# Kernel tuning notes

Hardware: AMD Instinct MI355X
Metric: run time of the kernel (lower is better)

The kernel has to match this reference:

```python
import jax, jax.numpy as jnp
import numpy as np

N_NODES = 100000
N_EDGES = 1600000
IN_CH = 128
HID = 128
OUT_CH = 2
NUM_GRAPHS = 512


def _mlp_params(key, d_in, d_out):
    k1, k2 = jax.random.split(key)
    s1 = 1.0 / np.sqrt(d_in)
    s2 = 1.0 / np.sqrt(d_out)
    return (jax.random.uniform(k1, (d_in, d_out), jnp.float32, -s1, s1),
            jnp.zeros((d_out,), jnp.float32),
            jax.random.uniform(k2, (d_out, d_out), jnp.float32, -s2, s2),
            jnp.zeros((d_out,), jnp.float32))


def setup_inputs() -> dict:
    key = jax.random.key(0)
    ks = jax.random.split(key, 8)
    x = jax.random.normal(ks[0], (N_NODES, IN_CH), jnp.float32)
    edge_index = jax.random.randint(ks[1], (2, N_EDGES), 0, N_NODES, jnp.int64)
    batch = jnp.sort(jax.random.randint(ks[2], (N_NODES,), 0, NUM_GRAPHS, jnp.int64))
    w1_0, b1_0, w2_0, b2_0 = _mlp_params(ks[3], IN_CH, HID)
    w1_1, b1_1, w2_1, b2_1 = _mlp_params(ks[4], HID, HID)
    w1_2, b1_2, w2_2, b2_2 = _mlp_params(ks[5], HID, HID)
    s = 1.0 / np.sqrt(HID)
    w_lin = jax.random.uniform(ks[6], (HID, OUT_CH), jnp.float32, -s, s)
    b_lin = jnp.zeros((OUT_CH,), jnp.float32)
    return {"x": x, "edge_index": edge_index, "batch": batch,
            "w1_0": w1_0, "b1_0": b1_0, "w2_0": w2_0, "b2_0": b2_0,
            "w1_1": w1_1, "b1_1": b1_1, "w2_1": w2_1, "b2_1": b2_1,
            "w1_2": w1_2, "b1_2": b1_2, "w2_2": w2_2, "b2_2": b2_2,
            "w_lin": w_lin, "b_lin": b_lin}


def _gin_conv(x, src, dst, w1, b1, w2, b2):
    # GINConv with eps=0: MLP(x + sum_{j in N(i)} x_j)
    agg = jax.ops.segment_sum(x[src], dst, num_segments=N_NODES)  # [N, d]
    h = x + agg
    h = jax.nn.relu(h @ w1 + b1)
    return h @ w2 + b2


def reference(x, edge_index, batch,
              w1_0, b1_0, w2_0, b2_0,
              w1_1, b1_1, w2_1, b2_1,
              w1_2, b1_2, w2_2, b2_2,
              w_lin, b_lin):
    src, dst = edge_index[0], edge_index[1]
    h = _gin_conv(x, src, dst, w1_0, b1_0, w2_0, b2_0)
    h = jax.nn.relu(h)
    h = jax.nn.relu(_gin_conv(h, src, dst, w1_1, b1_1, w2_1, b2_1))
    h = jax.nn.relu(h)  # forward applies relu twice after GIN1
    h = _gin_conv(h, src, dst, w1_2, b1_2, w2_2, b2_2)
    # global mean pool per graph
    sums = jax.ops.segment_sum(h, batch, num_segments=NUM_GRAPHS)  # [G, d]
    counts = jax.ops.segment_sum(jnp.ones((N_NODES,), h.dtype), batch,
                                 num_segments=NUM_GRAPHS)
    pooled = sums / jnp.maximum(counts, 1.0)[:, None]
    # dropout is identity in eval mode
    return pooled @ w_lin + b_lin  # [G, OUT_CH]
```

## Files before the change

kernel.cpp:

```cpp
#include <hip/hip_runtime.h>
#include <hip/hip_bf16.h>

#define N_NODES   100000
#define N_EDGES   1600000
#define IN_CH     128
#define HID       128
#define OUT_CH    2
#define NUM_GRAPHS 512

#define BKT_SHIFT 9
#define NB2 ((N_NODES + 511) >> BKT_SHIFT)
#define PB  200
#define CHUNK (N_EDGES / PB)

#define NCAST (N_NODES * IN_CH / 4 / 256)

typedef __attribute__((ext_vector_type(8))) short bf16x8;
typedef __attribute__((ext_vector_type(4))) float f32x4;
typedef unsigned int uint32;
typedef unsigned long long uint64;

static __device__ __forceinline__ float b2f(uint32 b) {
    return __uint_as_float(b << 16);
}
static __device__ __forceinline__ unsigned short f2b(float f) {
    uint32 u = __float_as_uint(f);
    u += 0x7fffu + ((u >> 16) & 1u);
    return (unsigned short)(u >> 16);
}
static __device__ __forceinline__ void acc8(float* a, int4 v) {
    uint32 x;
    x = (uint32)v.x; a[0] += __uint_as_float(x << 16); a[1] += __uint_as_float(x & 0xffff0000u);
    x = (uint32)v.y; a[2] += __uint_as_float(x << 16); a[3] += __uint_as_float(x & 0xffff0000u);
    x = (uint32)v.z; a[4] += __uint_as_float(x << 16); a[5] += __uint_as_float(x & 0xffff0000u);
    x = (uint32)v.w; a[6] += __uint_as_float(x << 16); a[7] += __uint_as_float(x & 0xffff0000u);
}

__global__ void k_front(const float* __restrict__ x, unsigned short* __restrict__ h,
                        const float* w0, const float* w1, const float* w2,
                        const float* w3, const float* w4, const float* w5,
                        unsigned short* __restrict__ wt,
                        const int* __restrict__ dst, int* __restrict__ histG) {
    __shared__ int hist[NB2];
    int bid = blockIdx.x, t = threadIdx.x;
    if (bid < NCAST) {
        int base = (bid * 256 + t) * 4;
        float4 v = *(const float4*)(x + base);
        ushort4 o;
        o.x = f2b(v.x); o.y = f2b(v.y); o.z = f2b(v.z); o.w = f2b(v.w);
        *(ushort4*)(h + base) = o;
    } else if (bid < NCAST + 6) {
        const float* ws[6] = {w0, w1, w2, w3, w4, w5};
        int wi = bid - NCAST;
        const float* w = ws[wi];
        unsigned short* o = wt + wi * 16384;
        for (int i = t; i < 16384; i += 256) {
            int k = i >> 7, n = i & 127;
            o[n * 128 + k] = f2b(w[i]);
        }
    } else {
        int blk = bid - NCAST - 6;
        for (int i = t; i < NB2; i += 256) hist[i] = 0;
        __syncthreads();
        int base = blk * CHUNK;
        for (int i = t; i < CHUNK; i += 256)
            atomicAdd(&hist[dst[base + i] >> BKT_SHIFT], 1);
        __syncthreads();
        for (int i = t; i < NB2; i += 256) histG[i * PB + blk] = hist[i];
    }
}

__global__ void k_scan1(const int* __restrict__ in, int* __restrict__ out,
                        int* __restrict__ bsum, int n) {
    __shared__ int sm[256];
    int b = blockIdx.x, t = threadIdx.x;
    int base = b * 1024 + t * 4;
    int v0 = 0, v1 = 0, v2 = 0, v3 = 0;
    if (base + 3 < n) {
        int4 q = *(const int4*)(in + base);
        v0 = q.x; v1 = q.y; v2 = q.z; v3 = q.w;
    } else {
        if (base + 0 < n) v0 = in[base + 0];
        if (base + 1 < n) v1 = in[base + 1];
        if (base + 2 < n) v2 = in[base + 2];
        if (base + 3 < n) v3 = in[base + 3];
    }
    int s = v0 + v1 + v2 + v3;
    sm[t] = s;
    __syncthreads();
    for (int off = 1; off < 256; off <<= 1) {
        int u = (t >= off) ? sm[t - off] : 0;
        __syncthreads();
        sm[t] += u;
        __syncthreads();
    }
    int p = (t == 0) ? 0 : sm[t - 1];
    int o0 = p, o1 = p + v0, o2 = o1 + v1, o3 = o2 + v2;
    if (base + 3 < n) {
        *(int4*)(out + base) = make_int4(o0, o1, o2, o3);
    } else {
        if (base + 0 < n) out[base + 0] = o0;
        if (base + 1 < n) out[base + 1] = o1;
        if (base + 2 < n) out[base + 2] = o2;
        if (base + 3 < n) out[base + 3] = o3;
    }
    if (t == 255) bsum[b] = s + ((t == 0) ? 0 : sm[t - 1]);
}

__global__ void k_scan3b(int* __restrict__ out, const int* __restrict__ bsum, int n) {
    __shared__ int add_s;
    int b = blockIdx.x, t = threadIdx.x;
    if (t == 0) {
        int s = 0;
        for (int i = 0; i < b; ++i) s += bsum[i];
        add_s = s;
    }
    __syncthreads();
    int add = add_s;
    int base = b * 1024 + t * 4;
    if (base + 3 < n) {
        int4 q = *(const int4*)(out + base);
        q.x += add; q.y += add; q.z += add; q.w += add;
        *(int4*)(out + base) = q;
    } else {
        for (int j = 0; j < 4; ++j)
            if (base + j < n) out[base + j] += add;
    }
}

__global__ void k_p3g(const int* __restrict__ ei, const int* __restrict__ baseG,
                      uint64* __restrict__ ebuf,
                      const int* __restrict__ batch, int* __restrict__ goff) {
    __shared__ int cur[NB2];
    int t = threadIdx.x, blk = blockIdx.x;
    if (blk >= PB) {
        int g = (blk - PB) * 512 + t;
        if (g <= NUM_GRAPHS) {
            int lo = 0, hi = N_NODES;
            while (lo < hi) {
                int mid = (lo + hi) >> 1;
                if (batch[mid] < g) lo = mid + 1; else hi = mid;
            }
            goff[g] = lo;
        }
        return;
    }
    for (int i = t; i < NB2; i += 512) cur[i] = baseG[i * PB + blk];
    __syncthreads();
    int base = blk * CHUNK;
    for (int i = t; i < CHUNK; i += 512) {
        int e = base + i;
        int src = ei[e];
        int dst = ei[N_EDGES + e];
        int pos = atomicAdd(&cur[dst >> BKT_SHIFT], 1);
        ebuf[pos] = ((uint64)(uint32)dst << 32) | (uint32)src;
    }
}

__global__ void k_p4(const uint64* __restrict__ ebuf, const int* __restrict__ baseG,
                     int* __restrict__ off, int* __restrict__ csr) {
    __shared__ int ldeg[512];
    __shared__ int lscan[512];
    __shared__ int lcur[512];
    int b = blockIdx.x, t = threadIdx.x;
    int node0 = b << BKT_SHIFT;
    int nn = min(512, N_NODES - node0);
    int e0 = baseG[b * PB];
    int e1 = (b == NB2 - 1) ? N_EDGES : baseG[(b + 1) * PB];
    ldeg[t] = 0;
    __syncthreads();
    for (int e = e0 + t; e < e1; e += 512) {
        int dst = (int)(ebuf[e] >> 32);
        atomicAdd(&ldeg[dst - node0], 1);
    }
    __syncthreads();
    lscan[t] = ldeg[t];
    __syncthreads();
    for (int o = 1; o < 512; o <<= 1) {
        int v = (t >= o) ? lscan[t - o] : 0;
        __syncthreads();
        lscan[t] += v;
        __syncthreads();
    }
    int excl = (t == 0) ? 0 : lscan[t - 1];
    lcur[t] = e0 + excl;
    if (t < nn) off[node0 + t] = e0 + excl;
    if (b == NB2 - 1 && t == 0) off[N_NODES] = N_EDGES;
    __syncthreads();
    for (int e = e0 + t; e < e1; e += 512) {
        uint64 pr = ebuf[e];
        int dst = (int)(pr >> 32);
        int pos = atomicAdd(&lcur[dst - node0], 1);
        csr[pos] = (int)(pr & 0xffffffffu);
    }
}

__global__ void k_agg(const unsigned short* __restrict__ h,
                      const int* __restrict__ off, const int* __restrict__ csr,
                      unsigned short* __restrict__ hs) {
    int wid = (blockIdx.x * 256 + threadIdx.x) >> 6;
    int lane = threadIdx.x & 63;
    if (wid >= N_NODES) return;
    int g = lane >> 4, sub = lane & 15;
    int e0 = off[wid], e1 = off[wid + 1];
    float a[8] = {0.f, 0.f, 0.f, 0.f, 0.f, 0.f, 0.f, 0.f};
    int e = e0 + g;
    for (; e + 12 < e1; e += 16) {
        int s0 = csr[e], s1 = csr[e + 4], s2 = csr[e + 8], s3 = csr[e + 12];
        int4 v0 = *(const int4*)(h + (size_t)s0 * 128 + sub * 8);
        int4 v1 = *(const int4*)(h + (size_t)s1 * 128 + sub * 8);
        int4 v2 = *(const int4*)(h + (size_t)s2 * 128 + sub * 8);
        int4 v3 = *(const int4*)(h + (size_t)s3 * 128 + sub * 8);
        acc8(a, v0); acc8(a, v1); acc8(a, v2); acc8(a, v3);
    }
    for (; e + 4 < e1; e += 8) {
        int s0 = csr[e];
        int s1 = csr[e + 4];
        int4 v0 = *(const int4*)(h + (size_t)s0 * 128 + sub * 8);
        int4 v1 = *(const int4*)(h + (size_t)s1 * 128 + sub * 8);
        acc8(a, v0);
        acc8(a, v1);
    }
    if (e < e1) {
        int s0 = csr[e];
        int4 v0 = *(const int4*)(h + (size_t)s0 * 128 + sub * 8);
        acc8(a, v0);
    }
#pragma unroll
    for (int j = 0; j < 8; ++j) {
        a[j] += __shfl_xor(a[j], 16);
        a[j] += __shfl_xor(a[j], 32);
    }
    if (g == 0) {
        int4 sv = *(const int4*)(h + (size_t)wid * 128 + sub * 8);
        acc8(a, sv);
        int4 o;
        o.x = (int)((uint32)f2b(a[0]) | ((uint32)f2b(a[1]) << 16));
        o.y = (int)((uint32)f2b(a[2]) | ((uint32)f2b(a[3]) << 16));
        o.z = (int)((uint32)f2b(a[4]) | ((uint32)f2b(a[5]) << 16));
        o.w = (int)((uint32)f2b(a[6]) | ((uint32)f2b(a[7]) << 16));
        *(int4*)(hs + (size_t)wid * 128 + sub * 8) = o;
    }
}

template<int OUTER_RELU>
__global__ void k_mlp(const unsigned short* __restrict__ hs,
                      const unsigned short* __restrict__ w1t, const float* __restrict__ b1,
                      const unsigned short* __restrict__ w2t, const float* __restrict__ b2,
                      unsigned short* __restrict__ ho) {
    __shared__ unsigned short T[32 * 128];
    int tid = threadIdx.x;
    int lane = tid & 63, wave = tid >> 6;
    int l15 = lane & 15, l4 = lane >> 4;
    int row0 = blockIdx.x * 32;
    int wn0 = wave * 32;

    bf16x8 w1f[2][4], w2f[2][4];
#pragma unroll
    for (int nt = 0; nt < 2; ++nt)
#pragma unroll
        for (int k = 0; k < 4; ++k) {
            int o = (wn0 + nt * 16 + l15) * 128 + k * 32 + l4 * 8;
            w1f[nt][k] = *(const bf16x8*)(w1t + o);
            w2f[nt][k] = *(const bf16x8*)(w2t + o);
        }
    float bias1[2] = { b1[wn0 + l15], b1[wn0 + 16 + l15] };
    float bias2[2] = { b2[wn0 + l15], b2[wn0 + 16 + l15] };

#pragma unroll
    for (int mt = 0; mt < 2; ++mt) {
        int arow = row0 + mt * 16 + l15;
        const unsigned short* ap = hs + (size_t)arow * 128 + l4 * 8;
        bf16x8 a0 = *(const bf16x8*)(ap);
        bf16x8 a1 = *(const bf16x8*)(ap + 32);
        bf16x8 a2 = *(const bf16x8*)(ap + 64);
        bf16x8 a3 = *(const bf16x8*)(ap + 96);
#pragma unroll
        for (int nt = 0; nt < 2; ++nt) {
            f32x4 acc = {0.f, 0.f, 0.f, 0.f};
            acc = __builtin_amdgcn_mfma_f32_16x16x32_bf16(a0, w1f[nt][0], acc, 0, 0, 0);
            acc = __builtin_amdgcn_mfma_f32_16x16x32_bf16(a1, w1f[nt][1], acc, 0, 0, 0);
            acc = __builtin_amdgcn_mfma_f32_16x16x32_bf16(a2, w1f[nt][2], acc, 0, 0, 0);
            acc = __builtin_amdgcn_mfma_f32_16x16x32_bf16(a3, w1f[nt][3], acc, 0, 0, 0);
#pragma unroll
            for (int j = 0; j < 4; ++j) {
                float v = fmaxf(acc[j] + bias1[nt], 0.f);
                int trow = mt * 16 + l4 * 4 + j;
                int tcol = wn0 + nt * 16 + l15;
                int byte = (trow * 256 + tcol * 2) ^ ((trow & 7) << 4);
                *(unsigned short*)((char*)T + byte) = f2b(v);
            }
        }
    }
    __syncthreads();

#pragma unroll
    for (int mt = 0; mt < 2; ++mt) {
        int trow = mt * 16 + l15;
        int sw = (trow & 7) << 4;
        int rb = trow * 256 + l4 * 16;
        bf16x8 t0 = *(const bf16x8*)((const char*)T + ((rb + 0)   ^ sw));
        bf16x8 t1 = *(const bf16x8*)((const char*)T + ((rb + 64)  ^ sw));
        bf16x8 t2 = *(const bf16x8*)((const char*)T + ((rb + 128) ^ sw));
        bf16x8 t3 = *(const bf16x8*)((const char*)T + ((rb + 192) ^ sw));
        __syncthreads();
#pragma unroll
        for (int nt = 0; nt < 2; ++nt) {
            f32x4 acc = {0.f, 0.f, 0.f, 0.f};
            acc = __builtin_amdgcn_mfma_f32_16x16x32_bf16(t0, w2f[nt][0], acc, 0, 0, 0);
            acc = __builtin_amdgcn_mfma_f32_16x16x32_bf16(t1, w2f[nt][1], acc, 0, 0, 0);
            acc = __builtin_amdgcn_mfma_f32_16x16x32_bf16(t2, w2f[nt][2], acc, 0, 0, 0);
            acc = __builtin_amdgcn_mfma_f32_16x16x32_bf16(t3, w2f[nt][3], acc, 0, 0, 0);
#pragma unroll
            for (int j = 0; j < 4; ++j) {
                float v = acc[j] + bias2[nt];
                if (OUTER_RELU) v = fmaxf(v, 0.f);
                int orow = mt * 16 + l4 * 4 + j;
                int ocol = wn0 + nt * 16 + l15;
                int byte = (orow * 256 + ocol * 2) ^ ((orow & 7) << 4);
                *(unsigned short*)((char*)T + byte) = f2b(v);
            }
        }
    }
    __syncthreads();

    for (int c = tid; c < 512; c += 256) {
        int r = c >> 4, cc = c & 15;
        int byte = (r * 256 + cc * 16) ^ ((r & 7) << 4);
        int4 v = *(const int4*)((const char*)T + byte);
        *(int4*)(ho + (size_t)(row0 + r) * 128 + cc * 8) = v;
    }
}

__global__ void k_pool(const unsigned short* __restrict__ h,
                       const int* __restrict__ goff,
                       const float* __restrict__ wl, const float* __restrict__ bl,
                       float* __restrict__ out) {
    __shared__ float sm[4][64][2];
    int g = blockIdx.x;
    int tid = threadIdx.x;
    int wave = tid >> 6, lane = tid & 63;
    int e0 = goff[g], e1 = goff[g + 1];
    int c2 = lane << 1;
    float s0 = 0.f, s1 = 0.f;
    int r = e0 + wave;
    for (; r + 4 < e1; r += 8) {
        uint32 v0 = *(const uint32*)(h + (size_t)r * 128 + c2);
        uint32 v1 = *(const uint32*)(h + (size_t)(r + 4) * 128 + c2);
        s0 += b2f(v0 & 0xffffu) + b2f(v1 & 0xffffu);
        s1 += b2f(v0 >> 16) + b2f(v1 >> 16);
    }
    if (r < e1) {
        uint32 v = *(const uint32*)(h + (size_t)r * 128 + c2);
        s0 += b2f(v & 0xffffu);
        s1 += b2f(v >> 16);
    }
    sm[wave][lane][0] = s0;
    sm[wave][lane][1] = s1;
    __syncthreads();
    if (wave == 0) {
        s0 = sm[0][lane][0] + sm[1][lane][0] + sm[2][lane][0] + sm[3][lane][0];
        s1 = sm[0][lane][1] + sm[1][lane][1] + sm[2][lane][1] + sm[3][lane][1];
        float inv = 1.f / fmaxf((float)(e1 - e0), 1.f);
        s0 *= inv; s1 *= inv;
        float o0 = s0 * wl[c2 * 2]     + s1 * wl[(c2 + 1) * 2];
        float o1 = s0 * wl[c2 * 2 + 1] + s1 * wl[(c2 + 1) * 2 + 1];
#pragma unroll
        for (int d = 32; d; d >>= 1) {
            o0 += __shfl_down(o0, d);
            o1 += __shfl_down(o1, d);
        }
        if (lane == 0) {
            out[g * 2]     = o0 + bl[0];
            out[g * 2 + 1] = o1 + bl[1];
        }
    }
}

extern "C" void kernel_launch(void* const* d_in, const int* in_sizes, int n_in,
                              void* d_out, int out_size, void* d_ws, size_t ws_size,
                              hipStream_t stream) {
    const float* x     = (const float*)d_in[0];
    const int*   ei    = (const int*)d_in[1];
    const int*   batch = (const int*)d_in[2];
    const float* w1[3] = {(const float*)d_in[3],  (const float*)d_in[7],  (const float*)d_in[11]};
    const float* b1[3] = {(const float*)d_in[4],  (const float*)d_in[8],  (const float*)d_in[12]};
    const float* w2[3] = {(const float*)d_in[5],  (const float*)d_in[9],  (const float*)d_in[13]};
    const float* b2[3] = {(const float*)d_in[6],  (const float*)d_in[10], (const float*)d_in[14]};
    const float* wl    = (const float*)d_in[15];
    const float* bl    = (const float*)d_in[16];

    char* p = (char*)d_ws;
    auto alloc = [&](size_t bytes) {
        char* r = p;
        p += (bytes + 255) & ~(size_t)255;
        return r;
    };
    int* off    = (int*)alloc((size_t)(N_NODES + 1) * 4);
    int* goff   = (int*)alloc((size_t)(NUM_GRAPHS + 1) * 4);
    int* histG  = (int*)alloc((size_t)(NB2 * PB) * 4);
    int* baseG  = (int*)alloc((size_t)(NB2 * PB + 1) * 4);
    int* bsum   = (int*)alloc((size_t)128 * 4);
    int* csr    = (int*)alloc((size_t)N_EDGES * 4);
    unsigned short* wts = (unsigned short*)alloc((size_t)6 * 16384 * 2);
    unsigned short* hA  = (unsigned short*)alloc((size_t)N_NODES * 128 * 2);
    unsigned short* hS  = (unsigned short*)alloc((size_t)N_NODES * 128 * 2);
    unsigned short* hB  = (unsigned short*)alloc((size_t)N_NODES * 128 * 2);
    uint64* ebuf = (uint64*)hS;

    k_front<<<NCAST + 6 + PB, 256, 0, stream>>>(x, hA,
        w1[0], w2[0], w1[1], w2[1], w1[2], w2[2], wts, ei + N_EDGES, histG);

    const int SCAN_N = NB2 * PB;
    const int SCAN_BLOCKS = (SCAN_N + 1023) / 1024;
    k_scan1<<<SCAN_BLOCKS, 256, 0, stream>>>(histG, baseG, bsum, SCAN_N);
    k_scan3b<<<SCAN_BLOCKS, 256, 0, stream>>>(baseG, bsum, SCAN_N);
    k_p3g<<<PB + 2, 512, 0, stream>>>(ei, baseG, ebuf, batch, goff);
    k_p4<<<NB2, 512, 0, stream>>>(ebuf, baseG, off, csr);

    unsigned short* wt1[3] = {wts,             wts + 2 * 16384, wts + 4 * 16384};
    unsigned short* wt2[3] = {wts + 1 * 16384, wts + 3 * 16384, wts + 5 * 16384};

    const int AGG_GRID = N_NODES / 4;
    const int MLP_GRID = N_NODES / 32;

    k_agg<<<AGG_GRID, 256, 0, stream>>>(hA, off, csr, hS);
    k_mlp<1><<<MLP_GRID, 256, 0, stream>>>(hS, wt1[0], b1[0], wt2[0], b2[0], hB);
    k_agg<<<AGG_GRID, 256, 0, stream>>>(hB, off, csr, hS);
    k_mlp<1><<<MLP_GRID, 256, 0, stream>>>(hS, wt1[1], b1[1], wt2[1], b2[1], hA);
    k_agg<<<AGG_GRID, 256, 0, stream>>>(hA, off, csr, hS);
    k_mlp<0><<<MLP_GRID, 256, 0, stream>>>(hS, wt1[2], b1[2], wt2[2], b2[2], hB);

    k_pool<<<NUM_GRAPHS, 256, 0, stream>>>(hB, goff, wl, bl, (float*)d_out);
}
```

Baseline: 375.9 us.

## Fuse neighbor aggregation into GIN MLP kernel via shared-memory tile

```diff
diff --git a/kernel.cpp b/kernel.cpp
--- a/kernel.cpp
+++ b/kernel.cpp
@@ -195,66 +195,64 @@
     }
 }
 
-__global__ void k_agg(const unsigned short* __restrict__ h,
+template<int OUTER_RELU>
+__global__ void k_gin(const unsigned short* __restrict__ h,
                       const int* __restrict__ off, const int* __restrict__ csr,
-                      unsigned short* __restrict__ hs) {
-    int wid = (blockIdx.x * 256 + threadIdx.x) >> 6;
-    int lane = threadIdx.x & 63;
-    if (wid >= N_NODES) return;
-    int g = lane >> 4, sub = lane & 15;
-    int e0 = off[wid], e1 = off[wid + 1];
-    float a[8] = {0.f, 0.f, 0.f, 0.f, 0.f, 0.f, 0.f, 0.f};
-    int e = e0 + g;
-    for (; e + 12 < e1; e += 16) {
-        int s0 = csr[e], s1 = csr[e + 4], s2 = csr[e + 8], s3 = csr[e + 12];
-        int4 v0 = *(const int4*)(h + (size_t)s0 * 128 + sub * 8);
-        int4 v1 = *(const int4*)(h + (size_t)s1 * 128 + sub * 8);
-        int4 v2 = *(const int4*)(h + (size_t)s2 * 128 + sub * 8);
-        int4 v3 = *(const int4*)(h + (size_t)s3 * 128 + sub * 8);
-        acc8(a, v0); acc8(a, v1); acc8(a, v2); acc8(a, v3);
-    }
-    for (; e + 4 < e1; e += 8) {
-        int s0 = csr[e];
-        int s1 = csr[e + 4];
-        int4 v0 = *(const int4*)(h + (size_t)s0 * 128 + sub * 8);
-        int4 v1 = *(const int4*)(h + (size_t)s1 * 128 + sub * 8);
-        acc8(a, v0);
-        acc8(a, v1);
-    }
-    if (e < e1) {
-        int s0 = csr[e];
-        int4 v0 = *(const int4*)(h + (size_t)s0 * 128 + sub * 8);
-        acc8(a, v0);
-    }
-#pragma unroll
-    for (int j = 0; j < 8; ++j) {
-        a[j] += __shfl_xor(a[j], 16);
-        a[j] += __shfl_xor(a[j], 32);
-    }
-    if (g == 0) {
-        int4 sv = *(const int4*)(h + (size_t)wid * 128 + sub * 8);
-        acc8(a, sv);
-        int4 o;
-        o.x = (int)((uint32)f2b(a[0]) | ((uint32)f2b(a[1]) << 16));
-        o.y = (int)((uint32)f2b(a[2]) | ((uint32)f2b(a[3]) << 16));
-        o.z = (int)((uint32)f2b(a[4]) | ((uint32)f2b(a[5]) << 16));
-        o.w = (int)((uint32)f2b(a[6]) | ((uint32)f2b(a[7]) << 16));
-        *(int4*)(hs + (size_t)wid * 128 + sub * 8) = o;
-    }
-}
-
-template<int OUTER_RELU>
-__global__ void k_mlp(const unsigned short* __restrict__ hs,
                       const unsigned short* __restrict__ w1t, const float* __restrict__ b1,
                       const unsigned short* __restrict__ w2t, const float* __restrict__ b2,
                       unsigned short* __restrict__ ho) {
-    __shared__ unsigned short T[32 * 128];
+    __shared__ unsigned short T[64 * 128];
     int tid = threadIdx.x;
     int lane = tid & 63, wave = tid >> 6;
     int l15 = lane & 15, l4 = lane >> 4;
-    int row0 = blockIdx.x * 32;
+    int row0 = blockIdx.x * 64;
+
+    int g = l4, sub = l15;
+    for (int r = wave * 16; r < wave * 16 + 16; ++r) {
+        int node = row0 + r;
+        if (node >= N_NODES) node = N_NODES - 1;
+        int e0 = off[node], e1 = off[node + 1];
+        float a[8] = {0.f, 0.f, 0.f, 0.f, 0.f, 0.f, 0.f, 0.f};
+        int e = e0 + g;
+        for (; e + 12 < e1; e += 16) {
+            int s0 = csr[e], s1 = csr[e + 4], s2 = csr[e + 8], s3 = csr[e + 12];
+            int4 v0 = *(const int4*)(h + (size_t)s0 * 128 + sub * 8);
+            int4 v1 = *(const int4*)(h + (size_t)s1 * 128 + sub * 8);
+            int4 v2 = *(const int4*)(h + (size_t)s2 * 128 + sub * 8);
+            int4 v3 = *(const int4*)(h + (size_t)s3 * 128 + sub * 8);
+            acc8(a, v0); acc8(a, v1); acc8(a, v2); acc8(a, v3);
+        }
+        for (; e + 4 < e1; e += 8) {
+            int s0 = csr[e], s1 = csr[e + 4];
+            int4 v0 = *(const int4*)(h + (size_t)s0 * 128 + sub * 8);
+            int4 v1 = *(const int4*)(h + (size_t)s1 * 128 + sub * 8);
+            acc8(a, v0); acc8(a, v1);
+        }
+        if (e < e1) {
+            int s0 = csr[e];
+            int4 v0 = *(const int4*)(h + (size_t)s0 * 128 + sub * 8);
+            acc8(a, v0);
+        }
+#pragma unroll
+        for (int j = 0; j < 8; ++j) {
+            a[j] += __shfl_xor(a[j], 16);
+            a[j] += __shfl_xor(a[j], 32);
+        }
+        if (g == 0) {
+            int4 sv = *(const int4*)(h + (size_t)node * 128 + sub * 8);
+            acc8(a, sv);
+            int4 o;
+            o.x = (int)((uint32)f2b(a[0]) | ((uint32)f2b(a[1]) << 16));
+            o.y = (int)((uint32)f2b(a[2]) | ((uint32)f2b(a[3]) << 16));
+            o.z = (int)((uint32)f2b(a[4]) | ((uint32)f2b(a[5]) << 16));
+            o.w = (int)((uint32)f2b(a[6]) | ((uint32)f2b(a[7]) << 16));
+            int byte = (r * 256 + sub * 16) ^ ((r & 7) << 4);
+            *(int4*)((char*)T + byte) = o;
+        }
+    }
+    __syncthreads();
+
     int wn0 = wave * 32;
-
     bf16x8 w1f[2][4], w2f[2][4];
 #pragma unroll
     for (int nt = 0; nt < 2; ++nt)
@@ -268,13 +266,15 @@
     float bias2[2] = { b2[wn0 + l15], b2[wn0 + 16 + l15] };
 
 #pragma unroll
-    for (int mt = 0; mt < 2; ++mt) {
-        int arow = row0 + mt * 16 + l15;
-        const unsigned short* ap = hs + (size_t)arow * 128 + l4 * 8;
-        bf16x8 a0 = *(const bf16x8*)(ap);
-        bf16x8 a1 = *(const bf16x8*)(ap + 32);
-        bf16x8 a2 = *(const bf16x8*)(ap + 64);
-        bf16x8 a3 = *(const bf16x8*)(ap + 96);
+    for (int mt = 0; mt < 4; ++mt) {
+        int trow = mt * 16 + l15;
+        int sw = (trow & 7) << 4;
+        int rb = trow * 256 + l4 * 16;
+        bf16x8 a0 = *(const bf16x8*)((const char*)T + ((rb + 0)   ^ sw));
+        bf16x8 a1 = *(const bf16x8*)((const char*)T + ((rb + 64)  ^ sw));
+        bf16x8 a2 = *(const bf16x8*)((const char*)T + ((rb + 128) ^ sw));
+        bf16x8 a3 = *(const bf16x8*)((const char*)T + ((rb + 192) ^ sw));
+        __syncthreads();
 #pragma unroll
         for (int nt = 0; nt < 2; ++nt) {
             f32x4 acc = {0.f, 0.f, 0.f, 0.f};
@@ -285,9 +285,9 @@
 #pragma unroll
             for (int j = 0; j < 4; ++j) {
                 float v = fmaxf(acc[j] + bias1[nt], 0.f);
-                int trow = mt * 16 + l4 * 4 + j;
-                int tcol = wn0 + nt * 16 + l15;
-                int byte = (trow * 256 + tcol * 2) ^ ((trow & 7) << 4);
+                int orow = mt * 16 + l4 * 4 + j;
+                int ocol = wn0 + nt * 16 + l15;
+                int byte = (orow * 256 + ocol * 2) ^ ((orow & 7) << 4);
                 *(unsigned short*)((char*)T + byte) = f2b(v);
             }
         }
@@ -295,7 +295,7 @@
     __syncthreads();
 
 #pragma unroll
-    for (int mt = 0; mt < 2; ++mt) {
+    for (int mt = 0; mt < 4; ++mt) {
         int trow = mt * 16 + l15;
         int sw = (trow & 7) << 4;
         int rb = trow * 256 + l4 * 16;
@@ -324,11 +324,13 @@
     }
     __syncthreads();
 
-    for (int c = tid; c < 512; c += 256) {
+    for (int c = tid; c < 1024; c += 256) {
         int r = c >> 4, cc = c & 15;
         int byte = (r * 256 + cc * 16) ^ ((r & 7) << 4);
         int4 v = *(const int4*)((const char*)T + byte);
-        *(int4*)(ho + (size_t)(row0 + r) * 128 + cc * 8) = v;
+        int gr = row0 + r;
+        if (gr < N_NODES)
+            *(int4*)(ho + (size_t)gr * 128 + cc * 8) = v;
     }
 }
 
@@ -421,15 +423,11 @@
     unsigned short* wt1[3] = {wts,             wts + 2 * 16384, wts + 4 * 16384};
     unsigned short* wt2[3] = {wts + 1 * 16384, wts + 3 * 16384, wts + 5 * 16384};
 
-    const int AGG_GRID = N_NODES / 4;
-    const int MLP_GRID = N_NODES / 32;
-
-    k_agg<<<AGG_GRID, 256, 0, stream>>>(hA, off, csr, hS);
-    k_mlp<1><<<MLP_GRID, 256, 0, stream>>>(hS, wt1[0], b1[0], wt2[0], b2[0], hB);
-    k_agg<<<AGG_GRID, 256, 0, stream>>>(hB, off, csr, hS);
-    k_mlp<1><<<MLP_GRID, 256, 0, stream>>>(hS, wt1[1], b1[1], wt2[1], b2[1], hA);
-    k_agg<<<AGG_GRID, 256, 0, stream>>>(hA, off, csr, hS);
-    k_mlp<0><<<MLP_GRID, 256, 0, stream>>>(hS, wt1[2], b1[2], wt2[2], b2[2], hB);
+    const int GIN_GRID = (N_NODES + 63) / 64;
+
+    k_gin<1><<<GIN_GRID, 256, 0, stream>>>(hA, off, csr, wt1[0], b1[0], wt2[0], b2[0], hB);
+    k_gin<1><<<GIN_GRID, 256, 0, stream>>>(hB, off, csr, wt1[1], b1[1], wt2[1], b2[1], hA);
+    k_gin<0><<<GIN_GRID, 256, 0, stream>>>(hA, off, csr, wt1[2], b1[2], wt2[2], b2[2], hB);
 
     k_pool<<<NUM_GRAPHS, 256, 0, stream>>>(hB, goff, wl, bl, (float*)d_out);
 }
```

After: 394.5 us. 1.05x slower.
